# Performance work log

Measured on AMD Instinct MI355X. Metric: run time of the kernel, lower is better.

Reference implementation:

```python
import jax, jax.numpy as jnp
import numpy as np

INPUT_SIZE = 512
HIDDEN_SIZE = 1024
SEQ_LEN = 512
BATCH = 64


def _xavier(key, shape):
    fan_out, fan_in = shape
    limit = float(np.sqrt(6.0 / (fan_in + fan_out)))
    return jax.random.uniform(key, shape, jnp.float32, -limit, limit)


def setup_inputs() -> dict:
    key = jax.random.key(0)
    ks = jax.random.split(key, 10)
    return {
        "x_seq": jax.random.normal(ks[0], (SEQ_LEN, BATCH, INPUT_SIZE), jnp.float32),
        "h": jax.random.normal(ks[1], (BATCH, HIDDEN_SIZE), jnp.float32),
        "U_c": _xavier(ks[2], (HIDDEN_SIZE, INPUT_SIZE)),
        "w_c": jax.random.normal(ks[3], (HIDDEN_SIZE,), jnp.float32),
        "b_c": jax.random.normal(ks[4], (HIDDEN_SIZE,), jnp.float32),
        "U_a": _xavier(ks[5], (HIDDEN_SIZE, INPUT_SIZE)),
        "w_a": jax.random.normal(ks[6], (HIDDEN_SIZE,), jnp.float32),
        "b_a": jax.random.normal(ks[7], (HIDDEN_SIZE,), jnp.float32),
        "U_h": _xavier(ks[8], (HIDDEN_SIZE, INPUT_SIZE)),
        "b_h": jax.random.normal(ks[9], (HIDDEN_SIZE,), jnp.float32),
    }


def reference(x_seq, h, U_c, w_c, b_c, U_a, w_a, b_a, U_h, b_h):
    # Precompute all input projections in one big batched GEMM each:
    # (S, B, I) @ (I, H) -> (S, B, H)
    xc = jnp.einsum("sbi,hi->sbh", x_seq, U_c) + b_c
    xa = jnp.einsum("sbi,hi->sbh", x_seq, U_a) + b_a
    xh = jnp.einsum("sbi,hi->sbh", x_seq, U_h) + b_h

    def step(h, proj):
        pc, pa, ph = proj
        c = jax.nn.sigmoid(pc + w_c * h)
        a = 1.0 + jnp.tanh(pa + w_a * h)
        h_new = c * h + (1.0 - c) * jnp.tanh(ph + a * h)
        return h_new, h_new

    hn, y_seq = jax.lax.scan(step, h, (xc, xa, xh))
    return y_seq, hn
```

## Files before the change

### kernel.cpp

```cpp
#include <hip/hip_runtime.h>
#include <hip/hip_bf16.h>
#include <stdint.h>

#define SEQLEN 512
#define NBATCH 64
#define KDIM   512
#define HDIM   1024
#define MTOT   (SEQLEN * NBATCH)
#define NTOT   (3 * HDIM)
#define STRIDE (NBATCH * HDIM)

typedef __attribute__((ext_vector_type(4))) float f32x4;
typedef _Float16 f16x8 __attribute__((ext_vector_type(8)));

__global__ __launch_bounds__(256) void cvt_x(const float* __restrict__ x,
                                             _Float16* __restrict__ xh,
                                             _Float16* __restrict__ xl) {
    int i = blockIdx.x * 256 + threadIdx.x;
    const float4* s = (const float4*)(x + (size_t)i * 8);
    float4 a = s[0], b = s[1];
    float v[8] = {a.x, a.y, a.z, a.w, b.x, b.y, b.z, b.w};
    f16x8 hi, lo;
#pragma unroll
    for (int j = 0; j < 8; ++j) {
        _Float16 h = (_Float16)v[j];
        hi[j] = h;
        lo[j] = (_Float16)(v[j] - (float)h);
    }
    *(f16x8*)(xh + (size_t)i * 8) = hi;
    *(f16x8*)(xl + (size_t)i * 8) = lo;
}

__global__ __launch_bounds__(256) void cvt_u(const float* __restrict__ Uc,
                                             const float* __restrict__ Ua,
                                             const float* __restrict__ Uh,
                                             _Float16* __restrict__ uh,
                                             _Float16* __restrict__ ul) {
    int i = blockIdx.x * 256 + threadIdx.x;
    int n = i >> 6;
    int kb = (i & 63) * 8;
    const float* src = (n < HDIM) ? (Uc + (size_t)n * KDIM)
                     : (n < 2 * HDIM) ? (Ua + (size_t)(n - HDIM) * KDIM)
                     : (Uh + (size_t)(n - 2 * HDIM) * KDIM);
    const float4* s = (const float4*)(src + kb);
    float4 a = s[0], b = s[1];
    float v[8] = {a.x, a.y, a.z, a.w, b.x, b.y, b.z, b.w};
    f16x8 hi, lo;
#pragma unroll
    for (int j = 0; j < 8; ++j) {
        _Float16 h = (_Float16)v[j];
        hi[j] = h;
        lo[j] = (_Float16)(v[j] - (float)h);
    }
    *(f16x8*)(uh + (size_t)n * KDIM + kb) = hi;
    *(f16x8*)(ul + (size_t)n * KDIM + kb) = lo;
}

#define BM 256
#define BN 256
#define BK 32
#define NT_N (NTOT / BN)
#define GRID ((MTOT / BM) * NT_N)
#define KT_N (KDIM / BK)

__device__ __forceinline__ void gload16(const _Float16* g, _Float16* l) {
    __builtin_amdgcn_global_load_lds((const __attribute__((address_space(1))) void*)g,
                                     (__attribute__((address_space(3))) void*)l,
                                     16, 0, 0);
}

__device__ __forceinline__ f32x4 mfma16(f16x8 a, f16x8 b, f32x4 c) {
    return __builtin_amdgcn_mfma_f32_16x16x32_f16(a, b, c, 0, 0, 0);
}

__global__ __launch_bounds__(512, 2) void gemm_f16x2(const _Float16* __restrict__ Ah,
                                                     const _Float16* __restrict__ Al,
                                                     const _Float16* __restrict__ Bh,
                                                     const _Float16* __restrict__ Bl,
                                                     float* __restrict__ pc,
                                                     float* __restrict__ pa,
                                                     float* __restrict__ ph) {
    __shared__ _Float16 lds[2][4][BM * BK];

    int bid  = blockIdx.x;
    int bm   = bid / NT_N;
    int bn   = bid % NT_N;
    int tid  = threadIdx.x;
    int lane = tid & 63;
    int wave = tid >> 6;
    int wr   = wave >> 2;
    int wc   = wave & 3;

    size_t row_off = (size_t)(tid >> 2) * KDIM
                   + (size_t)(((tid & 3) ^ ((tid >> 3) & 3)) * 8);
    const _Float16* gAh = Ah + (size_t)bm * BM * KDIM + row_off;
    const _Float16* gAl = Al + (size_t)bm * BM * KDIM + row_off;
    const _Float16* gBh = Bh + (size_t)bn * BN * KDIM + row_off;
    const _Float16* gBl = Bl + (size_t)bn * BN * KDIM + row_off;
    const size_t HPAN = (size_t)128 * KDIM;
    int t8 = tid * 8;

#define SPAIR(buf, plane, gp, kt) do { int _g = (kt) * BK;                     \
    gload16((gp) + _g,        &lds[buf][plane][t8]);                           \
    gload16((gp) + HPAN + _g, &lds[buf][plane][t8 + 4096]); } while (0)

    f32x4 acc[8][4];
#pragma unroll
    for (int i = 0; i < 8; ++i)
#pragma unroll
        for (int j = 0; j < 4; ++j)
            acc[i][j] = (f32x4){0.f, 0.f, 0.f, 0.f};

    int ro = lane & 15;
    int ko = ((lane >> 4) ^ ((lane >> 1) & 3)) * 8;

    f16x8 a_[4][2], b_[4][2];

#define READ_A(mh) _Pragma("unroll")                                           \
    for (int i = 0; i < 4; ++i) {                                              \
        int row = wr * 128 + ((mh) * 4 + i) * 16 + ro;                         \
        a_[i][0] = *(const f16x8*)(&lds[cur][0][row * BK + ko]);               \
        a_[i][1] = *(const f16x8*)(&lds[cur][1][row * BK + ko]);               \
    }
#define READ_B() _Pragma("unroll")                                             \
    for (int j = 0; j < 4; ++j) {                                              \
        int row = wc * 64 + j * 16 + ro;                                       \
        b_[j][0] = *(const f16x8*)(&lds[cur][2][row * BK + ko]);               \
        b_[j][1] = *(const f16x8*)(&lds[cur][3][row * BK + ko]);               \
    }
#define MFMA_HALF(mh) _Pragma("unroll")                                        \
    for (int i = 0; i < 4; ++i) _Pragma("unroll")                              \
        for (int j = 0; j < 4; ++j) {                                          \
            f32x4 c = acc[(mh) * 4 + i][j];                                    \
            c = mfma16(a_[i][0], b_[j][1], c);                      \
            c = mfma16(a_[i][1], b_[j][0], c);                      \
            c = mfma16(a_[i][0], b_[j][0], c);                      \
            acc[(mh) * 4 + i][j] = c;                                          \
        }

    SPAIR(0, 0, gAh, 0);
    SPAIR(0, 1, gAl, 0);
    SPAIR(0, 2, gBh, 0);
    SPAIR(0, 3, gBl, 0);

    for (int kt = 0; kt < KT_N; ++kt) {
        int cur = kt & 1, nxt = 1 - cur;
        bool pre = (kt < KT_N - 1);
        __builtin_amdgcn_sched_barrier(0);
        asm volatile("s_waitcnt vmcnt(0)" ::: "memory");
        __builtin_amdgcn_s_barrier();
        __builtin_amdgcn_sched_barrier(0);

        READ_B();
        READ_A(0);
        if (pre) { SPAIR(nxt, 0, gAh, kt + 1); SPAIR(nxt, 1, gAl, kt + 1); }
        __builtin_amdgcn_s_setprio(1);
        MFMA_HALF(0);
        __builtin_amdgcn_s_setprio(0);
        READ_A(1);
        if (pre) { SPAIR(nxt, 2, gBh, kt + 1); SPAIR(nxt, 3, gBl, kt + 1); }
        __builtin_amdgcn_s_setprio(1);
        MFMA_HALF(1);
        __builtin_amdgcn_s_setprio(0);
    }

    int n0 = bn * BN;
    float* outp; int nb;
    if (n0 < HDIM)            { outp = pc; nb = n0; }
    else if (n0 < 2 * HDIM)   { outp = pa; nb = n0 - HDIM; }
    else                      { outp = ph; nb = n0 - 2 * HDIM; }

#pragma unroll
    for (int ai = 0; ai < 8; ++ai)
#pragma unroll
        for (int bj = 0; bj < 4; ++bj) {
            int m = bm * BM + wr * 128 + ai * 16 + (lane >> 4) * 4;
            int n = nb + wc * 64 + bj * 16 + (lane & 15);
#pragma unroll
            for (int r = 0; r < 4; ++r)
                outp[(size_t)(m + r) * HDIM + n] = acc[ai][bj][r];
        }
#undef SPAIR
#undef READ_A
#undef READ_B
#undef MFMA_HALF
}

__global__ __launch_bounds__(256) void recur(const float* __restrict__ pc_a,
                                             const float* __restrict__ pa_a,
                                             float* out,
                                             const float* __restrict__ h0,
                                             const float* __restrict__ wc_,
                                             const float* __restrict__ bc_,
                                             const float* __restrict__ wa_,
                                             const float* __restrict__ ba_,
                                             const float* __restrict__ bh_) {
    int idx = blockIdx.x * 256 + threadIdx.x;
    int j = idx & (HDIM - 1);
    float h  = h0[idx];
    float wc = wc_[j], bc = bc_[j];
    float wa = wa_[j], ba = ba_[j];
    float bh = bh_[j];

#define PF 32
    float pc[PF], pa[PF], ph[PF];
#pragma unroll
    for (int u = 0; u < PF; ++u) {
        pc[u] = pc_a[(size_t)u * STRIDE + idx];
        pa[u] = pa_a[(size_t)u * STRIDE + idx];
        ph[u] = out [(size_t)u * STRIDE + idx];
    }

    for (int sb = 0; sb < SEQLEN; sb += PF) {
#pragma unroll
        for (int u = 0; u < PF; ++u) {
            int s = sb + u;
            float vc = pc[u], va = pa[u], vh = ph[u];
            int sp = s + PF; sp = (sp < SEQLEN) ? sp : (SEQLEN - 1);
            pc[u] = pc_a[(size_t)sp * STRIDE + idx];
            pa[u] = pa_a[(size_t)sp * STRIDE + idx];
            ph[u] = out [(size_t)sp * STRIDE + idx];

            float zc = (vc + bc) + wc * h;
            float za = (va + ba) + wa * h;
            float c  = 1.0f / (1.0f + expf(-zc));
            float a  = 1.0f + tanhf(za);
            float ht = tanhf((vh + bh) + a * h);
            h = c * h + (1.0f - c) * ht;
            out[(size_t)s * STRIDE + idx] = h;
        }
    }
    out[(size_t)SEQLEN * STRIDE + idx] = h;
}

extern "C" void kernel_launch(void* const* d_in, const int* in_sizes, int n_in,
                              void* d_out, int out_size, void* d_ws, size_t ws_size,
                              hipStream_t stream) {
    const float* x_seq = (const float*)d_in[0];
    const float* h0    = (const float*)d_in[1];
    const float* U_c   = (const float*)d_in[2];
    const float* w_c   = (const float*)d_in[3];
    const float* b_c   = (const float*)d_in[4];
    const float* U_a   = (const float*)d_in[5];
    const float* w_a   = (const float*)d_in[6];
    const float* b_a   = (const float*)d_in[7];
    const float* U_h   = (const float*)d_in[8];
    const float* b_h   = (const float*)d_in[9];
    float* out = (float*)d_out;

    char* ws = (char*)d_ws;
    const size_t MB = 1024 * 1024;
    float*    ws_pc = (float*)ws;
    float*    ws_pa = (float*)(ws + 128 * MB);
    _Float16* x_hi  = (_Float16*)(ws + 256 * MB);
    _Float16* x_lo  = (_Float16*)(ws + 288 * MB);
    _Float16* u_hi  = (_Float16*)(ws + 320 * MB);
    _Float16* u_lo  = (_Float16*)(ws + 323 * MB);

    cvt_x<<<dim3(MTOT * KDIM / 8 / 256), dim3(256), 0, stream>>>(x_seq, x_hi, x_lo);
    cvt_u<<<dim3(NTOT * KDIM / 8 / 256), dim3(256), 0, stream>>>(U_c, U_a, U_h, u_hi, u_lo);
    gemm_f16x2<<<dim3(GRID), dim3(512), 0, stream>>>(
        x_hi, x_lo, u_hi, u_lo, ws_pc, ws_pa, out);
    recur<<<dim3(STRIDE / 256), dim3(256), 0, stream>>>(ws_pc, ws_pa, out, h0,
                                                        w_c, b_c, w_a, b_a, b_h);
}
```

Measured before the change: 462.7 us.

## Shrink GEMM N-tile to 128 with triple-buffered LDS pipeline and reduce recurrence prefetch

The split-f16 GEMM tile shrinks from 256x256 to 256x128, with 8 waves arranged 4x2 and half the accumulators per wave. LDS goes from double to triple buffering so loads for kt+2 are in flight while computing kt, using a partial vmcnt wait. This is meant to cut register pressure and hide global latency better. The trade-off is lower data reuse per tile and more blocks. The recurrence prefetch depth also drops from 32 to 16 steps to relieve register use.

```diff
diff --git a/kernel.cpp b/kernel.cpp
--- a/kernel.cpp
+++ b/kernel.cpp
@@ -57,11 +57,16 @@
 }
 
 #define BM 256
-#define BN 256
+#define BN 128
 #define BK 32
 #define NT_N (NTOT / BN)
 #define GRID ((MTOT / BM) * NT_N)
 #define KT_N (KDIM / BK)
+#define OFF_AH 0
+#define OFF_AL 8192
+#define OFF_BH 16384
+#define OFF_BL 20480
+#define BUF_HW 24576
 
 __device__ __forceinline__ void gload16(const _Float16* g, _Float16* l) {
     __builtin_amdgcn_global_load_lds((const __attribute__((address_space(1))) void*)g,
@@ -80,7 +85,7 @@
                                                      float* __restrict__ pc,
                                                      float* __restrict__ pa,
                                                      float* __restrict__ ph) {
-    __shared__ _Float16 lds[2][4][BM * BK];
+    __shared__ _Float16 lds[3][BUF_HW];
 
     int bid  = blockIdx.x;
     int bm   = bid / NT_N;
@@ -88,8 +93,8 @@
     int tid  = threadIdx.x;
     int lane = tid & 63;
     int wave = tid >> 6;
-    int wr   = wave >> 2;
-    int wc   = wave & 3;
+    int wr   = wave >> 1;
+    int wc   = wave & 1;
 
     size_t row_off = (size_t)(tid >> 2) * KDIM
                    + (size_t)(((tid & 3) ^ ((tid >> 3) & 3)) * 8);
@@ -97,16 +102,20 @@
     const _Float16* gAl = Al + (size_t)bm * BM * KDIM + row_off;
     const _Float16* gBh = Bh + (size_t)bn * BN * KDIM + row_off;
     const _Float16* gBl = Bl + (size_t)bn * BN * KDIM + row_off;
-    const size_t HPAN = (size_t)128 * KDIM;
+    const size_t P128 = (size_t)128 * KDIM;
     int t8 = tid * 8;
 
-#define SPAIR(buf, plane, gp, kt) do { int _g = (kt) * BK;                     \
-    gload16((gp) + _g,        &lds[buf][plane][t8]);                           \
-    gload16((gp) + HPAN + _g, &lds[buf][plane][t8 + 4096]); } while (0)
-
-    f32x4 acc[8][4];
-#pragma unroll
-    for (int i = 0; i < 8; ++i)
+#define STAGE(buf, kt) do { int _g = (kt) * BK;                                \
+    gload16(gAh + _g,        &lds[buf][OFF_AH + t8]);                          \
+    gload16(gAh + P128 + _g, &lds[buf][OFF_AH + 4096 + t8]);                   \
+    gload16(gAl + _g,        &lds[buf][OFF_AL + t8]);                          \
+    gload16(gAl + P128 + _g, &lds[buf][OFF_AL + 4096 + t8]);                   \
+    gload16(gBh + _g,        &lds[buf][OFF_BH + t8]);                          \
+    gload16(gBl + _g,        &lds[buf][OFF_BL + t8]); } while (0)
+
+    f32x4 acc[4][4];
+#pragma unroll
+    for (int i = 0; i < 4; ++i)
 #pragma unroll
         for (int j = 0; j < 4; ++j)
             acc[i][j] = (f32x4){0.f, 0.f, 0.f, 0.f};
@@ -116,74 +125,67 @@
 
     f16x8 a_[4][2], b_[4][2];
 
-#define READ_A(mh) _Pragma("unroll")                                           \
+#define READ_A(cb) _Pragma("unroll")                                           \
     for (int i = 0; i < 4; ++i) {                                              \
-        int row = wr * 128 + ((mh) * 4 + i) * 16 + ro;                         \
-        a_[i][0] = *(const f16x8*)(&lds[cur][0][row * BK + ko]);               \
-        a_[i][1] = *(const f16x8*)(&lds[cur][1][row * BK + ko]);               \
-    }
-#define READ_B() _Pragma("unroll")                                             \
+        int row = wr * 64 + i * 16 + ro;                                       \
+        a_[i][0] = *(const f16x8*)(&lds[cb][OFF_AH + row * BK + ko]);          \
+        a_[i][1] = *(const f16x8*)(&lds[cb][OFF_AL + row * BK + ko]);          \
+    }
+#define READ_B(cb) _Pragma("unroll")                                           \
     for (int j = 0; j < 4; ++j) {                                              \
         int row = wc * 64 + j * 16 + ro;                                       \
-        b_[j][0] = *(const f16x8*)(&lds[cur][2][row * BK + ko]);               \
-        b_[j][1] = *(const f16x8*)(&lds[cur][3][row * BK + ko]);               \
-    }
-#define MFMA_HALF(mh) _Pragma("unroll")                                        \
+        b_[j][0] = *(const f16x8*)(&lds[cb][OFF_BH + row * BK + ko]);          \
+        b_[j][1] = *(const f16x8*)(&lds[cb][OFF_BL + row * BK + ko]);          \
+    }
+#define MFMA_ALL() _Pragma("unroll")                                           \
     for (int i = 0; i < 4; ++i) _Pragma("unroll")                              \
         for (int j = 0; j < 4; ++j) {                                          \
-            f32x4 c = acc[(mh) * 4 + i][j];                                    \
+            f32x4 c = acc[i][j];                                               \
             c = mfma16(a_[i][0], b_[j][1], c);                      \
             c = mfma16(a_[i][1], b_[j][0], c);                      \
             c = mfma16(a_[i][0], b_[j][0], c);                      \
-            acc[(mh) * 4 + i][j] = c;                                          \
+            acc[i][j] = c;                                                     \
         }
 
-    SPAIR(0, 0, gAh, 0);
-    SPAIR(0, 1, gAl, 0);
-    SPAIR(0, 2, gBh, 0);
-    SPAIR(0, 3, gBl, 0);
-
+    STAGE(0, 0);
+    STAGE(1, 1);
+
+    int c0 = 0, c1 = 1, c2 = 2;
     for (int kt = 0; kt < KT_N; ++kt) {
-        int cur = kt & 1, nxt = 1 - cur;
-        bool pre = (kt < KT_N - 1);
         __builtin_amdgcn_sched_barrier(0);
-        asm volatile("s_waitcnt vmcnt(0)" ::: "memory");
+        if (kt < KT_N - 1) asm volatile("s_waitcnt vmcnt(6)" ::: "memory");
+        else               asm volatile("s_waitcnt vmcnt(0)" ::: "memory");
         __builtin_amdgcn_s_barrier();
         __builtin_amdgcn_sched_barrier(0);
 
-        READ_B();
-        READ_A(0);
-        if (pre) { SPAIR(nxt, 0, gAh, kt + 1); SPAIR(nxt, 1, gAl, kt + 1); }
+        READ_B(c0);
+        READ_A(c0);
+        if (kt + 2 < KT_N) STAGE(c2, kt + 2);
         __builtin_amdgcn_s_setprio(1);
-        MFMA_HALF(0);
+        MFMA_ALL();
         __builtin_amdgcn_s_setprio(0);
-        READ_A(1);
-        if (pre) { SPAIR(nxt, 2, gBh, kt + 1); SPAIR(nxt, 3, gBl, kt + 1); }
-        __builtin_amdgcn_s_setprio(1);
-        MFMA_HALF(1);
-        __builtin_amdgcn_s_setprio(0);
+
+        int t = c0; c0 = c1; c1 = c2; c2 = t;
     }
 
     int n0 = bn * BN;
-    float* outp; int nb;
-    if (n0 < HDIM)            { outp = pc; nb = n0; }
-    else if (n0 < 2 * HDIM)   { outp = pa; nb = n0 - HDIM; }
-    else                      { outp = ph; nb = n0 - 2 * HDIM; }
-
-#pragma unroll
-    for (int ai = 0; ai < 8; ++ai)
-#pragma unroll
-        for (int bj = 0; bj < 4; ++bj) {
-            int m = bm * BM + wr * 128 + ai * 16 + (lane >> 4) * 4;
-            int n = nb + wc * 64 + bj * 16 + (lane & 15);
-#pragma unroll
-            for (int r = 0; r < 4; ++r)
-                outp[(size_t)(m + r) * HDIM + n] = acc[ai][bj][r];
+    float* outp = (n0 < HDIM) ? pc : (n0 < 2 * HDIM) ? pa : ph;
+    int nb = n0 & (HDIM - 1);
+#pragma unroll
+    for (int i = 0; i < 4; ++i)
+#pragma unroll
+        for (int r = 0; r < 4; ++r) {
+            int m = bm * BM + wr * 64 + i * 16 + (lane >> 4) * 4 + r;
+#pragma unroll
+            for (int j = 0; j < 4; ++j) {
+                int n = nb + wc * 64 + j * 16 + (lane & 15);
+                outp[(size_t)m * HDIM + n] = acc[i][j][r];
+            }
         }
-#undef SPAIR
+#undef STAGE
 #undef READ_A
 #undef READ_B
-#undef MFMA_HALF
+#undef MFMA_ALL
 }
 
 __global__ __launch_bounds__(256) void recur(const float* __restrict__ pc_a,
@@ -202,7 +204,7 @@
     float wa = wa_[j], ba = ba_[j];
     float bh = bh_[j];
 
-#define PF 32
+#define PF 16
     float pc[PF], pa[PF], ph[PF];
 #pragma unroll
     for (int u = 0; u < PF; ++u) {
```

New measurement: 514.7 us. 1.11x slower.

## Load low-part fp16 tiles directly to registers in MFMA fragment layout

Applied to the files above, without the earlier changes.

The conversion kernel now writes the low-order fp16 residuals of x and U in a pre-swizzled per-fragment layout, and the two conversion kernels are merged into one launch. The GEMM stages only the high parts through LDS, halving LDS traffic and footprint, and loads the low parts straight from global memory into registers, double-buffered across an unrolled pair of k-iterations. The recurrence prefetch depth drops from 32 to 16. This cuts LDS reads and occupancy pressure, at the cost of more registers and uncached-style global loads inside the MFMA loop.

```diff
diff --git a/kernel.cpp b/kernel.cpp
--- a/kernel.cpp
+++ b/kernel.cpp
@@ -13,11 +13,35 @@
 typedef __attribute__((ext_vector_type(4))) float f32x4;
 typedef _Float16 f16x8 __attribute__((ext_vector_type(8)));
 
-__global__ __launch_bounds__(256) void cvt_x(const float* __restrict__ x,
-                                             _Float16* __restrict__ xh,
-                                             _Float16* __restrict__ xl) {
+#define XTHREADS (MTOT * KDIM / 8)
+#define UTHREADS (NTOT * KDIM / 8)
+#define KT_N (KDIM / 32)
+
+__global__ __launch_bounds__(256) void cvt_all(const float* __restrict__ x,
+                                               const float* __restrict__ Uc,
+                                               const float* __restrict__ Ua,
+                                               const float* __restrict__ Uh,
+                                               _Float16* __restrict__ xh,
+                                               _Float16* __restrict__ xlf,
+                                               _Float16* __restrict__ uh,
+                                               _Float16* __restrict__ ulf) {
     int i = blockIdx.x * 256 + threadIdx.x;
-    const float4* s = (const float4*)(x + (size_t)i * 8);
+    const float* src;
+    _Float16 *dh, *dlf;
+    int row, kb;
+    if (i < XTHREADS) {
+        row = i >> 6; kb = (i & 63) * 8;
+        src = x + (size_t)i * 8;
+        dh = xh; dlf = xlf;
+    } else {
+        int u = i - XTHREADS;
+        row = u >> 6; kb = (u & 63) * 8;
+        src = ((row < HDIM) ? (Uc + (size_t)row * KDIM)
+             : (row < 2 * HDIM) ? (Ua + (size_t)(row - HDIM) * KDIM)
+             : (Uh + (size_t)(row - 2 * HDIM) * KDIM)) + kb;
+        dh = uh; dlf = ulf;
+    }
+    const float4* s = (const float4*)src;
     float4 a = s[0], b = s[1];
     float v[8] = {a.x, a.y, a.z, a.w, b.x, b.y, b.z, b.w};
     f16x8 hi, lo;
@@ -27,33 +51,10 @@
         hi[j] = h;
         lo[j] = (_Float16)(v[j] - (float)h);
     }
-    *(f16x8*)(xh + (size_t)i * 8) = hi;
-    *(f16x8*)(xl + (size_t)i * 8) = lo;
-}
-
-__global__ __launch_bounds__(256) void cvt_u(const float* __restrict__ Uc,
-                                             const float* __restrict__ Ua,
-                                             const float* __restrict__ Uh,
-                                             _Float16* __restrict__ uh,
-                                             _Float16* __restrict__ ul) {
-    int i = blockIdx.x * 256 + threadIdx.x;
-    int n = i >> 6;
-    int kb = (i & 63) * 8;
-    const float* src = (n < HDIM) ? (Uc + (size_t)n * KDIM)
-                     : (n < 2 * HDIM) ? (Ua + (size_t)(n - HDIM) * KDIM)
-                     : (Uh + (size_t)(n - 2 * HDIM) * KDIM);
-    const float4* s = (const float4*)(src + kb);
-    float4 a = s[0], b = s[1];
-    float v[8] = {a.x, a.y, a.z, a.w, b.x, b.y, b.z, b.w};
-    f16x8 hi, lo;
-#pragma unroll
-    for (int j = 0; j < 8; ++j) {
-        _Float16 h = (_Float16)v[j];
-        hi[j] = h;
-        lo[j] = (_Float16)(v[j] - (float)h);
-    }
-    *(f16x8*)(uh + (size_t)n * KDIM + kb) = hi;
-    *(f16x8*)(ul + (size_t)n * KDIM + kb) = lo;
+    *(f16x8*)(dh + (size_t)row * KDIM + kb) = hi;
+    int lane16 = (row & 15) + (((kb >> 3) & 3) << 4);
+    size_t lof = ((size_t)((row >> 4) * KT_N + (kb >> 5))) * 512 + lane16 * 8;
+    *(f16x8*)(dlf + lof) = lo;
 }
 
 #define BM 256
@@ -61,7 +62,9 @@
 #define BK 32
 #define NT_N (NTOT / BN)
 #define GRID ((MTOT / BM) * NT_N)
-#define KT_N (KDIM / BK)
+#define OFF_AH 0
+#define OFF_BH 8192
+#define BUF_HW 16384
 
 __device__ __forceinline__ void gload16(const _Float16* g, _Float16* l) {
     __builtin_amdgcn_global_load_lds((const __attribute__((address_space(1))) void*)g,
@@ -74,13 +77,13 @@
 }
 
 __global__ __launch_bounds__(512, 2) void gemm_f16x2(const _Float16* __restrict__ Ah,
-                                                     const _Float16* __restrict__ Al,
+                                                     const _Float16* __restrict__ Alo,
                                                      const _Float16* __restrict__ Bh,
-                                                     const _Float16* __restrict__ Bl,
+                                                     const _Float16* __restrict__ Blo,
                                                      float* __restrict__ pc,
                                                      float* __restrict__ pa,
                                                      float* __restrict__ ph) {
-    __shared__ _Float16 lds[2][4][BM * BK];
+    __shared__ _Float16 lds[2][BUF_HW];
 
     int bid  = blockIdx.x;
     int bm   = bid / NT_N;
@@ -94,15 +97,27 @@
     size_t row_off = (size_t)(tid >> 2) * KDIM
                    + (size_t)(((tid & 3) ^ ((tid >> 3) & 3)) * 8);
     const _Float16* gAh = Ah + (size_t)bm * BM * KDIM + row_off;
-    const _Float16* gAl = Al + (size_t)bm * BM * KDIM + row_off;
     const _Float16* gBh = Bh + (size_t)bn * BN * KDIM + row_off;
-    const _Float16* gBl = Bl + (size_t)bn * BN * KDIM + row_off;
-    const size_t HPAN = (size_t)128 * KDIM;
+    const size_t P128 = (size_t)128 * KDIM;
     int t8 = tid * 8;
 
-#define SPAIR(buf, plane, gp, kt) do { int _g = (kt) * BK;                     \
-    gload16((gp) + _g,        &lds[buf][plane][t8]);                           \
-    gload16((gp) + HPAN + _g, &lds[buf][plane][t8 + 4096]); } while (0)
+#define STAGE_A(buf, kt) do { int _g = (kt) * BK;                              \
+    gload16(gAh + _g,        &lds[buf][OFF_AH + t8]);                          \
+    gload16(gAh + P128 + _g, &lds[buf][OFF_AH + 4096 + t8]); } while (0)
+#define STAGE_B(buf, kt) do { int _g = (kt) * BK;                              \
+    gload16(gBh + _g,        &lds[buf][OFF_BH + t8]);                          \
+    gload16(gBh + P128 + _g, &lds[buf][OFF_BH + 4096 + t8]); } while (0)
+
+    const _Float16* aloB = Alo + (size_t)(bm * 16 + wr * 8) * KT_N * 512 + lane * 8;
+    const _Float16* bloB = Blo + (size_t)(bn * 16 + wc * 4) * KT_N * 512 + lane * 8;
+
+#define LOAD_LO(aS, bS, kt) do { _Pragma("unroll")                             \
+    for (int i = 0; i < 8; ++i)                                                \
+        aS[i] = *(const f16x8*)(aloB + ((size_t)i * KT_N + (kt)) * 512);       \
+    _Pragma("unroll")                                                          \
+    for (int j = 0; j < 4; ++j)                                                \
+        bS[j] = *(const f16x8*)(bloB + ((size_t)j * KT_N + (kt)) * 512);       \
+    } while (0)
 
     f32x4 acc[8][4];
 #pragma unroll
@@ -114,54 +129,56 @@
     int ro = lane & 15;
     int ko = ((lane >> 4) ^ ((lane >> 1) & 3)) * 8;
 
-    f16x8 a_[4][2], b_[4][2];
-
-#define READ_A(mh) _Pragma("unroll")                                           \
+    f16x8 a0_[4], a1_[4], bh_[4];
+    f16x8 aloX[8], bloX[4], aloY[8], bloY[4];
+
+#define READ_A(arr, mh, cb) _Pragma("unroll")                                  \
     for (int i = 0; i < 4; ++i) {                                              \
         int row = wr * 128 + ((mh) * 4 + i) * 16 + ro;                         \
-        a_[i][0] = *(const f16x8*)(&lds[cur][0][row * BK + ko]);               \
-        a_[i][1] = *(const f16x8*)(&lds[cur][1][row * BK + ko]);               \
-    }
-#define READ_B() _Pragma("unroll")                                             \
+        arr[i] = *(const f16x8*)(&lds[cb][OFF_AH + row * BK + ko]);            \
+    }
+#define READ_B(cb) _Pragma("unroll")                                           \
     for (int j = 0; j < 4; ++j) {                                              \
         int row = wc * 64 + j * 16 + ro;                                       \
-        b_[j][0] = *(const f16x8*)(&lds[cur][2][row * BK + ko]);               \
-        b_[j][1] = *(const f16x8*)(&lds[cur][3][row * BK + ko]);               \
-    }
-#define MFMA_HALF(mh) _Pragma("unroll")                                        \
+        bh_[j] = *(const f16x8*)(&lds[cb][OFF_BH + row * BK + ko]);            \
+    }
+#define MFMA_HALF(mh, aHi, aLo, bLo) _Pragma("unroll")                         \
     for (int i = 0; i < 4; ++i) _Pragma("unroll")                              \
         for (int j = 0; j < 4; ++j) {                                          \
             f32x4 c = acc[(mh) * 4 + i][j];                                    \
-            c = mfma16(a_[i][0], b_[j][1], c);                      \
-            c = mfma16(a_[i][1], b_[j][0], c);                      \
-            c = mfma16(a_[i][0], b_[j][0], c);                      \
+            c = mfma16(aHi[i], bLo[j], c);                          \
+            c = mfma16(aLo[(mh) * 4 + i], bh_[j], c);               \
+            c = mfma16(aHi[i], bh_[j], c);                          \
             acc[(mh) * 4 + i][j] = c;                                          \
         }
 
-    SPAIR(0, 0, gAh, 0);
-    SPAIR(0, 1, gAl, 0);
-    SPAIR(0, 2, gBh, 0);
-    SPAIR(0, 3, gBl, 0);
-
-    for (int kt = 0; kt < KT_N; ++kt) {
-        int cur = kt & 1, nxt = 1 - cur;
-        bool pre = (kt < KT_N - 1);
-        __builtin_amdgcn_sched_barrier(0);
-        asm volatile("s_waitcnt vmcnt(0)" ::: "memory");
-        __builtin_amdgcn_s_barrier();
-        __builtin_amdgcn_sched_barrier(0);
-
-        READ_B();
-        READ_A(0);
-        if (pre) { SPAIR(nxt, 0, gAh, kt + 1); SPAIR(nxt, 1, gAl, kt + 1); }
-        __builtin_amdgcn_s_setprio(1);
-        MFMA_HALF(0);
-        __builtin_amdgcn_s_setprio(0);
-        READ_A(1);
-        if (pre) { SPAIR(nxt, 2, gBh, kt + 1); SPAIR(nxt, 3, gBl, kt + 1); }
-        __builtin_amdgcn_s_setprio(1);
-        MFMA_HALF(1);
-        __builtin_amdgcn_s_setprio(0);
+#define BODY(kt, LOA, LOB, NXA, NXB) do {                                      \
+    int cur = (kt) & 1, nxt = 1 - cur;                                         \
+    bool pre = ((kt) < KT_N - 1);                                              \
+    __builtin_amdgcn_sched_barrier(0);                                         \
+    asm volatile("s_waitcnt vmcnt(0)" ::: "memory");                           \
+    __builtin_amdgcn_s_barrier();                                              \
+    __builtin_amdgcn_sched_barrier(0);                                         \
+    if (pre) LOAD_LO(NXA, NXB, (kt) + 1);      \
+    READ_B(cur);                                                               \
+    READ_A(a0_, 0, cur);                                                       \
+    if (pre) STAGE_A(nxt, (kt) + 1);                                           \
+    __builtin_amdgcn_s_setprio(1);                                             \
+    MFMA_HALF(0, a0_, LOA, LOB);                                               \
+    __builtin_amdgcn_s_setprio(0);                                             \
+    READ_A(a1_, 1, cur);                                                       \
+    if (pre) STAGE_B(nxt, (kt) + 1);                                           \
+    __builtin_amdgcn_s_setprio(1);                                             \
+    MFMA_HALF(1, a1_, LOA, LOB);                                               \
+    __builtin_amdgcn_s_setprio(0);                                             \
+} while (0)
+
+    STAGE_A(0, 0); STAGE_B(0, 0);
+    LOAD_LO(aloX, bloX, 0);
+
+    for (int kt = 0; kt < KT_N; kt += 2) {
+        BODY(kt,     aloX, bloX, aloY, bloY);
+        BODY(kt + 1, aloY, bloY, aloX, bloX);
     }
 
     int n0 = bn * BN;
@@ -180,10 +197,13 @@
             for (int r = 0; r < 4; ++r)
                 outp[(size_t)(m + r) * HDIM + n] = acc[ai][bj][r];
         }
-#undef SPAIR
+#undef STAGE_A
+#undef STAGE_B
+#undef LOAD_LO
 #undef READ_A
 #undef READ_B
 #undef MFMA_HALF
+#undef BODY
 }
 
 __global__ __launch_bounds__(256) void recur(const float* __restrict__ pc_a,
@@ -202,7 +222,7 @@
     float wa = wa_[j], ba = ba_[j];
     float bh = bh_[j];
 
-#define PF 32
+#define PF 16
     float pc[PF], pa[PF], ph[PF];
 #pragma unroll
     for (int u = 0; u < PF; ++u) {
@@ -253,14 +273,14 @@
     float*    ws_pc = (float*)ws;
     float*    ws_pa = (float*)(ws + 128 * MB);
     _Float16* x_hi  = (_Float16*)(ws + 256 * MB);
-    _Float16* x_lo  = (_Float16*)(ws + 288 * MB);
+    _Float16* x_lof = (_Float16*)(ws + 288 * MB);
     _Float16* u_hi  = (_Float16*)(ws + 320 * MB);
-    _Float16* u_lo  = (_Float16*)(ws + 323 * MB);
-
-    cvt_x<<<dim3(MTOT * KDIM / 8 / 256), dim3(256), 0, stream>>>(x_seq, x_hi, x_lo);
-    cvt_u<<<dim3(NTOT * KDIM / 8 / 256), dim3(256), 0, stream>>>(U_c, U_a, U_h, u_hi, u_lo);
+    _Float16* u_lof = (_Float16*)(ws + 323 * MB);
+
+    cvt_all<<<dim3((XTHREADS + UTHREADS) / 256), dim3(256), 0, stream>>>(
+        x_seq, U_c, U_a, U_h, x_hi, x_lof, u_hi, u_lof);
     gemm_f16x2<<<dim3(GRID), dim3(512), 0, stream>>>(
-        x_hi, x_lo, u_hi, u_lo, ws_pc, ws_pa, out);
+        x_hi, x_lof, u_hi, u_lof, ws_pc, ws_pa, out);
     recur<<<dim3(STRIDE / 256), dim3(256), 0, stream>>>(ws_pc, ws_pa, out, h0,
                                                         w_c, b_c, w_a, b_a, b_h);
 }
```

Result: slower. 793.0 us (+71.4%).

## Interleave pc/pa projections for two timesteps into float4 and merge conversion kernels

Applied to the files above, without the earlier changes.

The GEMM epilogue now writes the c and a projections interleaved as float4 groups (pc/pa for steps 2k and 2k+1), so the recurrence kernel loads one 16-byte vector per two timesteps instead of four scalar loads, and processes two steps per iteration. The two fp16 split conversion kernels are fused into a single launch. This aims to cut load instruction count and launch overhead in the latency-bound recurrence, at the cost of 8-byte strided scattered stores in the GEMM epilogue.

```diff
diff --git a/kernel.cpp b/kernel.cpp
--- a/kernel.cpp
+++ b/kernel.cpp
@@ -10,14 +10,39 @@
 #define NTOT   (3 * HDIM)
 #define STRIDE (NBATCH * HDIM)
 
+typedef __attribute__((ext_vector_type(2))) float f32x2;
 typedef __attribute__((ext_vector_type(4))) float f32x4;
 typedef _Float16 f16x8 __attribute__((ext_vector_type(8)));
 
-__global__ __launch_bounds__(256) void cvt_x(const float* __restrict__ x,
-                                             _Float16* __restrict__ xh,
-                                             _Float16* __restrict__ xl) {
+#define XTHREADS (MTOT * KDIM / 8)
+#define UTHREADS (NTOT * KDIM / 8)
+__global__ __launch_bounds__(256) void cvt_all(const float* __restrict__ x,
+                                               const float* __restrict__ Uc,
+                                               const float* __restrict__ Ua,
+                                               const float* __restrict__ Uh,
+                                               _Float16* __restrict__ xh,
+                                               _Float16* __restrict__ xl,
+                                               _Float16* __restrict__ uh,
+                                               _Float16* __restrict__ ul) {
     int i = blockIdx.x * 256 + threadIdx.x;
-    const float4* s = (const float4*)(x + (size_t)i * 8);
+    const float* src;
+    _Float16 *dh, *dl;
+    size_t off;
+    if (i < XTHREADS) {
+        src = x + (size_t)i * 8;
+        off = (size_t)i * 8;
+        dh = xh; dl = xl;
+    } else {
+        int u = i - XTHREADS;
+        int n = u >> 6;
+        int kb = (u & 63) * 8;
+        src = ((n < HDIM) ? (Uc + (size_t)n * KDIM)
+             : (n < 2 * HDIM) ? (Ua + (size_t)(n - HDIM) * KDIM)
+             : (Uh + (size_t)(n - 2 * HDIM) * KDIM)) + kb;
+        off = (size_t)n * KDIM + kb;
+        dh = uh; dl = ul;
+    }
+    const float4* s = (const float4*)src;
     float4 a = s[0], b = s[1];
     float v[8] = {a.x, a.y, a.z, a.w, b.x, b.y, b.z, b.w};
     f16x8 hi, lo;
@@ -27,33 +52,8 @@
         hi[j] = h;
         lo[j] = (_Float16)(v[j] - (float)h);
     }
-    *(f16x8*)(xh + (size_t)i * 8) = hi;
-    *(f16x8*)(xl + (size_t)i * 8) = lo;
-}
-
-__global__ __launch_bounds__(256) void cvt_u(const float* __restrict__ Uc,
-                                             const float* __restrict__ Ua,
-                                             const float* __restrict__ Uh,
-                                             _Float16* __restrict__ uh,
-                                             _Float16* __restrict__ ul) {
-    int i = blockIdx.x * 256 + threadIdx.x;
-    int n = i >> 6;
-    int kb = (i & 63) * 8;
-    const float* src = (n < HDIM) ? (Uc + (size_t)n * KDIM)
-                     : (n < 2 * HDIM) ? (Ua + (size_t)(n - HDIM) * KDIM)
-                     : (Uh + (size_t)(n - 2 * HDIM) * KDIM);
-    const float4* s = (const float4*)(src + kb);
-    float4 a = s[0], b = s[1];
-    float v[8] = {a.x, a.y, a.z, a.w, b.x, b.y, b.z, b.w};
-    f16x8 hi, lo;
-#pragma unroll
-    for (int j = 0; j < 8; ++j) {
-        _Float16 h = (_Float16)v[j];
-        hi[j] = h;
-        lo[j] = (_Float16)(v[j] - (float)h);
-    }
-    *(f16x8*)(uh + (size_t)n * KDIM + kb) = hi;
-    *(f16x8*)(ul + (size_t)n * KDIM + kb) = lo;
+    *(f16x8*)(dh + off) = hi;
+    *(f16x8*)(dl + off) = lo;
 }
 
 #define BM 256
@@ -77,9 +77,8 @@
                                                      const _Float16* __restrict__ Al,
                                                      const _Float16* __restrict__ Bh,
                                                      const _Float16* __restrict__ Bl,
-                                                     float* __restrict__ pc,
-                                                     float* __restrict__ pa,
-                                                     float* __restrict__ ph) {
+                                                     float* __restrict__ pcpa,
+                                                     float* __restrict__ out) {
     __shared__ _Float16 lds[2][4][BM * BK];
 
     int bid  = blockIdx.x;
@@ -97,12 +96,12 @@
     const _Float16* gAl = Al + (size_t)bm * BM * KDIM + row_off;
     const _Float16* gBh = Bh + (size_t)bn * BN * KDIM + row_off;
     const _Float16* gBl = Bl + (size_t)bn * BN * KDIM + row_off;
-    const size_t HPAN = (size_t)128 * KDIM;
+    const size_t P128 = (size_t)128 * KDIM;
     int t8 = tid * 8;
 
 #define SPAIR(buf, plane, gp, kt) do { int _g = (kt) * BK;                     \
     gload16((gp) + _g,        &lds[buf][plane][t8]);                           \
-    gload16((gp) + HPAN + _g, &lds[buf][plane][t8 + 4096]); } while (0)
+    gload16((gp) + P128 + _g, &lds[buf][plane][t8 + 4096]); } while (0)
 
     f32x4 acc[8][4];
 #pragma unroll
@@ -138,10 +137,8 @@
             acc[(mh) * 4 + i][j] = c;                                          \
         }
 
-    SPAIR(0, 0, gAh, 0);
-    SPAIR(0, 1, gAl, 0);
-    SPAIR(0, 2, gBh, 0);
-    SPAIR(0, 3, gBl, 0);
+    SPAIR(0, 0, gAh, 0); SPAIR(0, 1, gAl, 0);
+    SPAIR(0, 2, gBh, 0); SPAIR(0, 3, gBl, 0);
 
     for (int kt = 0; kt < KT_N; ++kt) {
         int cur = kt & 1, nxt = 1 - cur;
@@ -165,29 +162,42 @@
     }
 
     int n0 = bn * BN;
-    float* outp; int nb;
-    if (n0 < HDIM)            { outp = pc; nb = n0; }
-    else if (n0 < 2 * HDIM)   { outp = pa; nb = n0 - HDIM; }
-    else                      { outp = ph; nb = n0 - 2 * HDIM; }
-
-#pragma unroll
-    for (int ai = 0; ai < 8; ++ai)
-#pragma unroll
-        for (int bj = 0; bj < 4; ++bj) {
-            int m = bm * BM + wr * 128 + ai * 16 + (lane >> 4) * 4;
-            int n = nb + wc * 64 + bj * 16 + (lane & 15);
-#pragma unroll
-            for (int r = 0; r < 4; ++r)
-                outp[(size_t)(m + r) * HDIM + n] = acc[ai][bj][r];
-        }
+    if (n0 < 2 * HDIM) {
+        int c = (n0 < HDIM) ? 0 : 2;
+        int nb = n0 & (HDIM - 1);
+        size_t prow = (size_t)(bm * 2 + wr) * (4 * STRIDE);
+#pragma unroll
+        for (int al = 0; al < 4; ++al)
+#pragma unroll
+            for (int bj = 0; bj < 4; ++bj) {
+                int n = nb + wc * 64 + bj * 16 + (lane & 15);
+#pragma unroll
+                for (int r = 0; r < 4; ++r) {
+                    int b = al * 16 + (lane >> 4) * 4 + r;
+                    f32x2 v = {acc[al][bj][r], acc[al + 4][bj][r]};
+                    *(f32x2*)(pcpa + prow + (size_t)(b * HDIM + n) * 4 + c) = v;
+                }
+            }
+    } else {
+        int nb = n0 - 2 * HDIM;
+#pragma unroll
+        for (int ai = 0; ai < 8; ++ai)
+#pragma unroll
+            for (int bj = 0; bj < 4; ++bj) {
+                int m = bm * BM + wr * 128 + ai * 16 + (lane >> 4) * 4;
+                int n = nb + wc * 64 + bj * 16 + (lane & 15);
+#pragma unroll
+                for (int r = 0; r < 4; ++r)
+                    out[(size_t)(m + r) * HDIM + n] = acc[ai][bj][r];
+            }
+    }
 #undef SPAIR
 #undef READ_A
 #undef READ_B
 #undef MFMA_HALF
 }
 
-__global__ __launch_bounds__(256) void recur(const float* __restrict__ pc_a,
-                                             const float* __restrict__ pa_a,
+__global__ __launch_bounds__(256) void recur(const float* __restrict__ pcpa,
                                              float* out,
                                              const float* __restrict__ h0,
                                              const float* __restrict__ wc_,
@@ -202,35 +212,51 @@
     float wa = wa_[j], ba = ba_[j];
     float bh = bh_[j];
 
-#define PF 32
-    float pc[PF], pa[PF], ph[PF];
-#pragma unroll
-    for (int u = 0; u < PF; ++u) {
-        pc[u] = pc_a[(size_t)u * STRIDE + idx];
-        pa[u] = pa_a[(size_t)u * STRIDE + idx];
-        ph[u] = out [(size_t)u * STRIDE + idx];
-    }
-
-    for (int sb = 0; sb < SEQLEN; sb += PF) {
-#pragma unroll
-        for (int u = 0; u < PF; ++u) {
-            int s = sb + u;
-            float vc = pc[u], va = pa[u], vh = ph[u];
-            int sp = s + PF; sp = (sp < SEQLEN) ? sp : (SEQLEN - 1);
-            pc[u] = pc_a[(size_t)sp * STRIDE + idx];
-            pa[u] = pa_a[(size_t)sp * STRIDE + idx];
-            ph[u] = out [(size_t)sp * STRIDE + idx];
-
-            float zc = (vc + bc) + wc * h;
-            float za = (va + ba) + wa * h;
+    const f32x4* PP = (const f32x4*)pcpa;
+
+#define NP 16
+    f32x4 pp[NP];
+    float ph[2 * NP];
+#pragma unroll
+    for (int u = 0; u < NP; ++u) {
+        pp[u] = PP[(size_t)u * STRIDE + idx];
+        ph[2 * u]     = out[(size_t)(2 * u) * STRIDE + idx];
+        ph[2 * u + 1] = out[(size_t)(2 * u + 1) * STRIDE + idx];
+    }
+
+    for (int sb = 0; sb < SEQLEN; sb += 2 * NP) {
+#pragma unroll
+        for (int u = 0; u < NP; ++u) {
+            int s = sb + 2 * u;
+            float vc0 = pp[u][0], vc1 = pp[u][1];
+            float va0 = pp[u][2], va1 = pp[u][3];
+            float vh0 = ph[2 * u], vh1 = ph[2 * u + 1];
+
+            int pn = (sb >> 1) + u + NP; pn = (pn < SEQLEN / 2) ? pn : (SEQLEN / 2 - 1);
+            pp[u] = PP[(size_t)pn * STRIDE + idx];
+            int sp0 = s + 2 * NP;     sp0 = (sp0 < SEQLEN) ? sp0 : (SEQLEN - 1);
+            int sp1 = s + 2 * NP + 1; sp1 = (sp1 < SEQLEN) ? sp1 : (SEQLEN - 1);
+            ph[2 * u]     = out[(size_t)sp0 * STRIDE + idx];
+            ph[2 * u + 1] = out[(size_t)sp1 * STRIDE + idx];
+
+            float zc = (vc0 + bc) + wc * h;
+            float za = (va0 + ba) + wa * h;
             float c  = 1.0f / (1.0f + expf(-zc));
             float a  = 1.0f + tanhf(za);
-            float ht = tanhf((vh + bh) + a * h);
+            float ht = tanhf((vh0 + bh) + a * h);
             h = c * h + (1.0f - c) * ht;
             out[(size_t)s * STRIDE + idx] = h;
+            zc = (vc1 + bc) + wc * h;
+            za = (va1 + ba) + wa * h;
+            c  = 1.0f / (1.0f + expf(-zc));
+            a  = 1.0f + tanhf(za);
+            ht = tanhf((vh1 + bh) + a * h);
+            h = c * h + (1.0f - c) * ht;
+            out[(size_t)(s + 1) * STRIDE + idx] = h;
         }
     }
     out[(size_t)SEQLEN * STRIDE + idx] = h;
+#undef NP
 }
 
 extern "C" void kernel_launch(void* const* d_in, const int* in_sizes, int n_in,
@@ -250,17 +276,16 @@
 
     char* ws = (char*)d_ws;
     const size_t MB = 1024 * 1024;
-    float*    ws_pc = (float*)ws;
-    float*    ws_pa = (float*)(ws + 128 * MB);
+    float*    ws_pcpa = (float*)ws;
     _Float16* x_hi  = (_Float16*)(ws + 256 * MB);
     _Float16* x_lo  = (_Float16*)(ws + 288 * MB);
     _Float16* u_hi  = (_Float16*)(ws + 320 * MB);
     _Float16* u_lo  = (_Float16*)(ws + 323 * MB);
 
-    cvt_x<<<dim3(MTOT * KDIM / 8 / 256), dim3(256), 0, stream>>>(x_seq, x_hi, x_lo);
-    cvt_u<<<dim3(NTOT * KDIM / 8 / 256), dim3(256), 0, stream>>>(U_c, U_a, U_h, u_hi, u_lo);
+    cvt_all<<<dim3((XTHREADS + UTHREADS) / 256), dim3(256), 0, stream>>>(
+        x_seq, U_c, U_a, U_h, x_hi, x_lo, u_hi, u_lo);
     gemm_f16x2<<<dim3(GRID), dim3(512), 0, stream>>>(
-        x_hi, x_lo, u_hi, u_lo, ws_pc, ws_pa, out);
-    recur<<<dim3(STRIDE / 256), dim3(256), 0, stream>>>(ws_pc, ws_pa, out, h0,
+        x_hi, x_lo, u_hi, u_lo, ws_pcpa, out);
+    recur<<<dim3(STRIDE / 256), dim3(256), 0, stream>>>(ws_pcpa, out, h0,
                                                         w_c, b_c, w_a, b_a, b_h);
 }
```

Measured after the change: 537.0 us. 16.1% more time.
